# Kernel tuning notes

Measured on AMD Instinct MI355X. Metric: run time of the kernel, lower is better.

Reference implementation:

```python
import jax, jax.numpy as jnp
import numpy as np

EMBED = 1024
DFF = 4096


def _layernorm(x, g, b, eps=1e-5):
    mu = jnp.mean(x, axis=-1, keepdims=True)
    var = jnp.var(x, axis=-1, keepdims=True)
    return (x - mu) * jax.lax.rsqrt(var + eps) * g + b


def setup_inputs() -> dict:
    key = jax.random.key(0)
    ks = jax.random.split(key, 14)
    s = 1.0 / np.sqrt(EMBED)
    sf = 1.0 / np.sqrt(DFF)
    d = {
        "src": jax.random.normal(ks[0], (4, 2048, EMBED), dtype=jnp.float32),
        "Wq": jax.random.uniform(ks[1], (EMBED, EMBED), jnp.float32, -s, s),
        "bq": jnp.zeros((EMBED,), jnp.float32),
        "Wk": jax.random.uniform(ks[2], (EMBED, EMBED), jnp.float32, -s, s),
        "bk": jnp.zeros((EMBED,), jnp.float32),
        "Wv": jax.random.uniform(ks[3], (EMBED, EMBED), jnp.float32, -s, s),
        "bv": jnp.zeros((EMBED,), jnp.float32),
        "Wo": jax.random.uniform(ks[4], (EMBED, EMBED), jnp.float32, -s, s),
        "bo": jnp.zeros((EMBED,), jnp.float32),
        "W1": jax.random.uniform(ks[5], (EMBED, DFF), jnp.float32, -s, s),
        "b1": jnp.zeros((DFF,), jnp.float32),
        "W2": jax.random.uniform(ks[6], (DFF, EMBED), jnp.float32, -sf, sf),
        "b2": jnp.zeros((EMBED,), jnp.float32),
        "g1": jnp.ones((EMBED,), jnp.float32),
        "be1": jnp.zeros((EMBED,), jnp.float32),
        "g2": jnp.ones((EMBED,), jnp.float32),
        "be2": jnp.zeros((EMBED,), jnp.float32),
    }
    return d


def reference(src, Wq, bq, Wk, bk, Wv, bv, Wo, bo, W1, b1, W2, b2, g1, be1, g2, be2):
    # Q/K/V projections: [b, s, d]
    Q = src @ Wq + bq
    K = src @ Wk + bk
    V = src @ Wv + bv
    # Single-head, UNSCALED attention (faithful to source: no 1/sqrt(d), num_heads unused)
    scores = jnp.einsum("bqd,bkd->bqk", Q, K)  # [b, s, s]
    weights = jax.nn.softmax(scores, axis=-1)
    attn = jnp.einsum("bqk,bkd->bqd", weights, V)
    attn = attn @ Wo + bo
    x = _layernorm(src + attn, g1, be1)
    ff = jax.nn.relu(x @ W1 + b1) @ W2 + b2
    return _layernorm(x + ff, g2, be2)
```

## Files before the change

kernel.cpp:

```cpp
#include <hip/hip_runtime.h>
#include <stdint.h>

typedef unsigned short u16;
typedef _Float16 v8h __attribute__((ext_vector_type(8)));
typedef float v4f __attribute__((ext_vector_type(4)));

static __device__ __forceinline__ float h2f(u16 u) {
    union { u16 s; _Float16 h; } v; v.s = u; return (float)v.h;
}
static __device__ __forceinline__ u16 f2h(float f) {
    union { u16 s; _Float16 h; } v; v.h = (_Float16)f; return v.s;
}

static __device__ __forceinline__ void gload_lds16(const u16* g, const u16* l) {
    __builtin_amdgcn_global_load_lds(
        (const __attribute__((address_space(1))) uint32_t*)(uintptr_t)g,
        (__attribute__((address_space(3))) uint32_t*)(uintptr_t)l,
        16, 0, 0);
}

__global__ __launch_bounds__(256) void cvt_f16(const float* __restrict__ in,
                                               u16* __restrict__ out, int n8) {
    const int i = blockIdx.x * 256 + threadIdx.x;
    if (i >= n8) return;
    const float4 a = ((const float4*)in)[2 * i];
    const float4 b = ((const float4*)in)[2 * i + 1];
    u16 o[8] = {f2h(a.x), f2h(a.y), f2h(a.z), f2h(a.w),
                f2h(b.x), f2h(b.y), f2h(b.z), f2h(b.w)};
    *(uint4*)(out + (size_t)i * 8) = *(const uint4*)o;
}

__global__ __launch_bounds__(256) void transpose_all(
    const float* __restrict__ Wq, const float* __restrict__ Wk,
    const float* __restrict__ Wv, const float* __restrict__ Wo,
    const float* __restrict__ W1, const float* __restrict__ W2,
    u16* __restrict__ WqkT, u16* __restrict__ WvT, u16* __restrict__ WoT,
    u16* __restrict__ W1T, u16* __restrict__ W2T)
{
    int t = blockIdx.x;
    const float* in; u16* out; long ldi, ldo; int xt;
    if (t < 1024)      {            in = Wq; out = WqkT;              ldi = 1024; ldo = 1024; xt = 32; }
    else if (t < 2048) { t -= 1024; in = Wk; out = WqkT + 1024*1024;  ldi = 1024; ldo = 1024; xt = 32; }
    else if (t < 3072) { t -= 2048; in = Wv; out = WvT;               ldi = 1024; ldo = 1024; xt = 32; }
    else if (t < 4096) { t -= 3072; in = Wo; out = WoT;               ldi = 1024; ldo = 1024; xt = 32; }
    else if (t < 8192) { t -= 4096; in = W1; out = W1T;               ldi = 4096; ldo = 1024; xt = 128; }
    else               { t -= 8192; in = W2; out = W2T;               ldi = 1024; ldo = 4096; xt = 32; }
    const int c0 = (t % xt) * 32, r0 = (t / xt) * 32;
    __shared__ float tile[32][33];
    for (int i = threadIdx.y; i < 32; i += 8)
        tile[i][threadIdx.x] = in[(long)(r0 + i) * ldi + c0 + threadIdx.x];
    __syncthreads();
    for (int i = threadIdx.y; i < 32; i += 8)
        out[(long)(c0 + i) * ldo + r0 + threadIdx.x] = f2h(tile[threadIdx.x][i]);
}

template<int OMODE, int BIAS, bool RELU>
__global__ __launch_bounds__(256) void gemm_f16(
    const u16* __restrict__ A, long lda, long Asb,
    const u16* __restrict__ B, long ldb, long Bsb,
    void* __restrict__ Cv, long ldc, long Csb,
    const float* __restrict__ bias, const float* __restrict__ bias2, int K)
{
    alignas(16) __shared__ u16 As[128 * 64];
    alignas(16) __shared__ u16 Bs[128 * 64];
    const int t = threadIdx.x;
    const long b = blockIdx.z;
    A += b * Asb; B += b * Bsb;
    const long m0 = (long)blockIdx.y * 128;
    const long n0 = (long)blockIdx.x * 128;
    const int lane = t & 63, wave = t >> 6;
    const int wm = (wave >> 1) * 64, wn = (wave & 1) * 64;
    const int l16 = lane & 15, quad = lane >> 4;

    const int rr = t >> 3;
    const int cg8 = ((t & 7) ^ ((t >> 3) & 7)) * 8;
    const int wv512 = wave * 512;

    long aofs[4], bofs[4];
#pragma unroll
    for (int p = 0; p < 4; ++p) {
        aofs[p] = (m0 + p * 32 + rr) * lda + cg8;
        bofs[p] = (n0 + p * 32 + rr) * ldb + cg8;
    }

    v4f acc[4][4];
#pragma unroll
    for (int i = 0; i < 4; ++i)
#pragma unroll
        for (int j = 0; j < 4; ++j)
            acc[i][j] = (v4f){0.f, 0.f, 0.f, 0.f};

    for (int k0 = 0; k0 < K; k0 += 64) {
        __syncthreads();
#pragma unroll
        for (int p = 0; p < 4; ++p) {
            gload_lds16(A + aofs[p] + k0, As + p * 2048 + wv512);
            gload_lds16(B + bofs[p] + k0, Bs + p * 2048 + wv512);
        }
        __syncthreads();

#pragma unroll
        for (int kk = 0; kk < 2; ++kk) {
            const int swz = ((kk * 4 + quad) ^ (l16 & 7)) * 8;
            v8h af[4], bfr[4];
#pragma unroll
            for (int i = 0; i < 4; ++i)
                af[i] = *(const v8h*)&As[(wm + i * 16 + l16) * 64 + swz];
#pragma unroll
            for (int j = 0; j < 4; ++j)
                bfr[j] = *(const v8h*)&Bs[(wn + j * 16 + l16) * 64 + swz];
#pragma unroll
            for (int i = 0; i < 4; ++i)
#pragma unroll
                for (int j = 0; j < 4; ++j)
                    acc[i][j] = __builtin_amdgcn_mfma_f32_16x16x32_f16(af[i], bfr[j], acc[i][j], 0, 0, 0);
        }
    }

    float bv[4];
#pragma unroll
    for (int j = 0; j < 4; ++j) {
        const long col = n0 + wn + j * 16 + l16;
        bv[j] = (BIAS == 0) ? 0.f
              : (BIAS == 1) ? bias[col]
              : (col < 1024 ? bias[col] : bias2[col - 1024]);
    }

    if (OMODE == 2) {
        const long bb = m0 >> 11, mb = m0 & 2047;
        u16* C = (u16*)Cv + bb * Csb;
#pragma unroll
        for (int j = 0; j < 4; ++j) {
            const long col = n0 + wn + j * 16 + l16;
            u16* pc = C + col * ldc + mb + wm + quad * 4;
#pragma unroll
            for (int i = 0; i < 4; ++i) {
                u16 o[4];
#pragma unroll
                for (int r = 0; r < 4; ++r) {
                    float val = acc[i][j][r] + bv[j];
                    if (RELU) val = fmaxf(val, 0.f);
                    o[r] = f2h(val);
                }
                *(uint2*)(pc + i * 16) = *(const uint2*)o;
            }
        }
    } else {
        const long cb = b * Csb + (m0 + wm + quad * 4) * ldc + (n0 + wn + l16);
        if (OMODE == 1) {
            float* p0 = (float*)Cv + cb;
#pragma unroll
            for (int i = 0; i < 4; ++i)
#pragma unroll
                for (int r = 0; r < 4; ++r) {
                    float* prow = p0 + (long)(i * 16 + r) * ldc;
#pragma unroll
                    for (int j = 0; j < 4; ++j) {
                        float val = acc[i][j][r] + bv[j];
                        if (RELU) val = fmaxf(val, 0.f);
                        prow[j * 16] = val;
                    }
                }
        } else {
            u16* p0 = (u16*)Cv + cb;
#pragma unroll
            for (int i = 0; i < 4; ++i)
#pragma unroll
                for (int r = 0; r < 4; ++r) {
                    u16* prow = p0 + (long)(i * 16 + r) * ldc;
#pragma unroll
                    for (int j = 0; j < 4; ++j) {
                        float val = acc[i][j][r] + bv[j];
                        if (RELU) val = fmaxf(val, 0.f);
                        prow[j * 16] = f2h(val);
                    }
                }
        }
    }
}

__global__ __launch_bounds__(256) void softmax_rows(float* __restrict__ S) {
    const long row = blockIdx.x;
    float* p = S + row * 2048;
    const int t = threadIdx.x;
    float v[8];
    float mx = -1e30f;
#pragma unroll
    for (int i = 0; i < 8; ++i) { v[i] = p[t + i * 256]; mx = fmaxf(mx, v[i]); }
    __shared__ float red[256];
    red[t] = mx; __syncthreads();
    for (int off = 128; off > 0; off >>= 1) {
        if (t < off) red[t] = fmaxf(red[t], red[t + off]);
        __syncthreads();
    }
    mx = red[0]; __syncthreads();
    float sum = 0.f;
#pragma unroll
    for (int i = 0; i < 8; ++i) { v[i] = __expf(v[i] - mx); sum += v[i]; }
    red[t] = sum; __syncthreads();
    for (int off = 128; off > 0; off >>= 1) {
        if (t < off) red[t] += red[t + off];
        __syncthreads();
    }
    const float inv = 1.f / red[0];
    u16* q = (u16*)p;
#pragma unroll
    for (int i = 0; i < 8; ++i) q[t + i * 256] = f2h(v[i] * inv);
}

__global__ __launch_bounds__(256) void ln_dual(
    const float* __restrict__ a, const u16* __restrict__ bb,
    const float* __restrict__ g, const float* __restrict__ be,
    float* __restrict__ out32, u16* __restrict__ out16)
{
    const long base = (long)blockIdx.x * 1024;
    const int t = threadIdx.x;
    float v[4]; float s = 0.f, ss = 0.f;
#pragma unroll
    for (int i = 0; i < 4; ++i) {
        const int c = t + i * 256;
        const float x = a[base + c] + h2f(bb[base + c]);
        v[i] = x; s += x; ss += x * x;
    }
    __shared__ float rs[256], rss[256];
    rs[t] = s; rss[t] = ss; __syncthreads();
    for (int off = 128; off > 0; off >>= 1) {
        if (t < off) { rs[t] += rs[t + off]; rss[t] += rss[t + off]; }
        __syncthreads();
    }
    const float mean = rs[0] * (1.f / 1024.f);
    const float var = rss[0] * (1.f / 1024.f) - mean * mean;
    const float rstd = rsqrtf(var + 1e-5f);
#pragma unroll
    for (int i = 0; i < 4; ++i) {
        const int c = t + i * 256;
        const float y = (v[i] - mean) * rstd * g[c] + be[c];
        out32[base + c] = y;
        out16[base + c] = f2h(y);
    }
}

__global__ __launch_bounds__(256) void ln_mix(
    const float* __restrict__ a, const u16* __restrict__ bb,
    const float* __restrict__ g, const float* __restrict__ be,
    float* __restrict__ out)
{
    const long base = (long)blockIdx.x * 1024;
    const int t = threadIdx.x;
    float v[4]; float s = 0.f, ss = 0.f;
#pragma unroll
    for (int i = 0; i < 4; ++i) {
        const int c = t + i * 256;
        const float x = a[base + c] + h2f(bb[base + c]);
        v[i] = x; s += x; ss += x * x;
    }
    __shared__ float rs[256], rss[256];
    rs[t] = s; rss[t] = ss; __syncthreads();
    for (int off = 128; off > 0; off >>= 1) {
        if (t < off) { rs[t] += rs[t + off]; rss[t] += rss[t + off]; }
        __syncthreads();
    }
    const float mean = rs[0] * (1.f / 1024.f);
    const float var = rss[0] * (1.f / 1024.f) - mean * mean;
    const float rstd = rsqrtf(var + 1e-5f);
#pragma unroll
    for (int i = 0; i < 4; ++i) {
        const int c = t + i * 256;
        out[base + c] = (v[i] - mean) * rstd * g[c] + be[c];
    }
}

extern "C" void kernel_launch(void* const* d_in, const int* in_sizes, int n_in,
                              void* d_out, int out_size, void* d_ws, size_t ws_size,
                              hipStream_t stream) {
    (void)in_sizes; (void)n_in; (void)out_size; (void)ws_size;
    constexpr long S = 2048, E = 1024, F = 4096, M = 8192;

    const float* src = (const float*)d_in[0];
    const float* Wq  = (const float*)d_in[1];
    const float* bq  = (const float*)d_in[2];
    const float* Wk  = (const float*)d_in[3];
    const float* bk  = (const float*)d_in[4];
    const float* Wv  = (const float*)d_in[5];
    const float* bv  = (const float*)d_in[6];
    const float* Wo  = (const float*)d_in[7];
    const float* bo  = (const float*)d_in[8];
    const float* W1  = (const float*)d_in[9];
    const float* b1  = (const float*)d_in[10];
    const float* W2  = (const float*)d_in[11];
    const float* b2  = (const float*)d_in[12];
    const float* g1  = (const float*)d_in[13];
    const float* be1 = (const float*)d_in[14];
    const float* g2  = (const float*)d_in[15];
    const float* be2 = (const float*)d_in[16];

    char* ws = (char*)d_ws;
    size_t off = 0;
    auto take = [&](size_t bytes) {
        char* p = ws + off;
        off += (bytes + 255) & ~(size_t)255;
        return p;
    };
    const size_t MB16 = 16777216;
    u16*   srcH  = (u16*)take(MB16);
    u16*   WqkT  = (u16*)take(2 * E * E * 2);
    u16*   WvT   = (u16*)take(E * E * 2);
    u16*   WoT   = (u16*)take(E * E * 2);
    u16*   W1T   = (u16*)take(F * E * 2);
    u16*   W2T   = (u16*)take(E * F * 2);
    char*  B0    = take(2 * MB16);
    char*  B1    = take(MB16);
    char*  B2    = take(4ull * S * S * 4);
    char*  B3    = take(MB16);
    char*  B4    = take(MB16);

    u16*   QK    = (u16*)B0;
    float* x32   = (float*)B0;
    u16*   VT    = (u16*)B1;
    float* Sf    = (float*)B2;
    u16*   hf    = (u16*)B2;
    u16*   attn  = (u16*)B3;
    u16*   xh    = (u16*)B3;
    u16*   attnO = (u16*)B4;
    u16*   ffO   = (u16*)B4;

    dim3 blk(256), tb(32, 8);

    cvt_f16<<<dim3(M * E / 8 / 256), blk, 0, stream>>>(src, srcH, M * E / 8);

    transpose_all<<<dim3(12288), tb, 0, stream>>>(Wq, Wk, Wv, Wo, W1, W2,
                                                  WqkT, WvT, WoT, W1T, W2T);

    gemm_f16<0, 2, false><<<dim3(16, 64, 1), blk, 0, stream>>>(
        srcH, E, 0, WqkT, E, 0, QK, 2 * E, 0, bq, bk, E);

    gemm_f16<2, 1, false><<<dim3(8, 64, 1), blk, 0, stream>>>(
        srcH, E, 0, WvT, E, 0, VT, S, E * S, bv, nullptr, E);

    gemm_f16<1, 0, false><<<dim3(16, 16, 4), blk, 0, stream>>>(
        QK, 2 * E, S * 2 * E, QK + E, 2 * E, S * 2 * E,
        Sf, S, S * S, nullptr, nullptr, E);

    softmax_rows<<<dim3(M), blk, 0, stream>>>(Sf);

    gemm_f16<0, 0, false><<<dim3(8, 16, 4), blk, 0, stream>>>(
        (const u16*)Sf, 2 * S, S * 2 * S, VT, S, E * S,
        attn, E, S * E, nullptr, nullptr, S);

    gemm_f16<0, 1, false><<<dim3(8, 64, 1), blk, 0, stream>>>(
        attn, E, 0, WoT, E, 0, attnO, E, 0, bo, nullptr, E);

    ln_dual<<<dim3(M), blk, 0, stream>>>(src, attnO, g1, be1, x32, xh);

    gemm_f16<0, 1, true><<<dim3(32, 64, 1), blk, 0, stream>>>(
        xh, E, 0, W1T, E, 0, hf, F, 0, b1, nullptr, E);

    gemm_f16<0, 1, false><<<dim3(8, 64, 1), blk, 0, stream>>>(
        hf, F, 0, W2T, F, 0, ffO, E, 0, b2, nullptr, F);

    ln_mix<<<dim3(M), blk, 0, stream>>>(x32, ffO, g2, be2, (float*)d_out);
}
```

Before: 558.1 us.

## Fuse QKV projection GEMM, store scores in fp16, drop fp32 LN intermediate

Merges the Q/K and V projection GEMMs into one launch over a concatenated QKV weight, with the V tiles written transposed through a second output pointer. Attention scores are now written as fp16 instead of fp32, so the score buffer traffic and the softmax read are halved. The first layernorm no longer writes an fp32 copy, and the second layernorm reads the fp16 residual instead. The cost is lower precision for the unscaled scores, where fp16 may lose accuracy or overflow, and for the residual path.

```diff
diff --git a/kernel.cpp b/kernel.cpp
--- a/kernel.cpp
+++ b/kernel.cpp
@@ -34,17 +34,17 @@
     const float* __restrict__ Wq, const float* __restrict__ Wk,
     const float* __restrict__ Wv, const float* __restrict__ Wo,
     const float* __restrict__ W1, const float* __restrict__ W2,
-    u16* __restrict__ WqkT, u16* __restrict__ WvT, u16* __restrict__ WoT,
+    u16* __restrict__ WqkvT, u16* __restrict__ WoT,
     u16* __restrict__ W1T, u16* __restrict__ W2T)
 {
     int t = blockIdx.x;
     const float* in; u16* out; long ldi, ldo; int xt;
-    if (t < 1024)      {            in = Wq; out = WqkT;              ldi = 1024; ldo = 1024; xt = 32; }
-    else if (t < 2048) { t -= 1024; in = Wk; out = WqkT + 1024*1024;  ldi = 1024; ldo = 1024; xt = 32; }
-    else if (t < 3072) { t -= 2048; in = Wv; out = WvT;               ldi = 1024; ldo = 1024; xt = 32; }
-    else if (t < 4096) { t -= 3072; in = Wo; out = WoT;               ldi = 1024; ldo = 1024; xt = 32; }
-    else if (t < 8192) { t -= 4096; in = W1; out = W1T;               ldi = 4096; ldo = 1024; xt = 128; }
-    else               { t -= 8192; in = W2; out = W2T;               ldi = 1024; ldo = 4096; xt = 32; }
+    if (t < 1024)      {            in = Wq; out = WqkvT;               ldi = 1024; ldo = 1024; xt = 32; }
+    else if (t < 2048) { t -= 1024; in = Wk; out = WqkvT + 1024*1024;   ldi = 1024; ldo = 1024; xt = 32; }
+    else if (t < 3072) { t -= 2048; in = Wv; out = WqkvT + 2*1024*1024; ldi = 1024; ldo = 1024; xt = 32; }
+    else if (t < 4096) { t -= 3072; in = Wo; out = WoT;                 ldi = 1024; ldo = 1024; xt = 32; }
+    else if (t < 8192) { t -= 4096; in = W1; out = W1T;                 ldi = 4096; ldo = 1024; xt = 128; }
+    else               { t -= 8192; in = W2; out = W2T;                 ldi = 1024; ldo = 4096; xt = 32; }
     const int c0 = (t % xt) * 32, r0 = (t / xt) * 32;
     __shared__ float tile[32][33];
     for (int i = threadIdx.y; i < 32; i += 8)
@@ -58,8 +58,9 @@
 __global__ __launch_bounds__(256) void gemm_f16(
     const u16* __restrict__ A, long lda, long Asb,
     const u16* __restrict__ B, long ldb, long Bsb,
-    void* __restrict__ Cv, long ldc, long Csb,
-    const float* __restrict__ bias, const float* __restrict__ bias2, int K)
+    void* __restrict__ Cv, long ldc, long Csb, u16* __restrict__ C1,
+    const float* __restrict__ bias, const float* __restrict__ bias2,
+    const float* __restrict__ bias3, int K)
 {
     alignas(16) __shared__ u16 As[128 * 64];
     alignas(16) __shared__ u16 Bs[128 * 64];
@@ -121,18 +122,22 @@
 #pragma unroll
     for (int j = 0; j < 4; ++j) {
         const long col = n0 + wn + j * 16 + l16;
-        bv[j] = (BIAS == 0) ? 0.f
-              : (BIAS == 1) ? bias[col]
-              : (col < 1024 ? bias[col] : bias2[col - 1024]);
-    }
-
-    if (OMODE == 2) {
+        if (BIAS == 0) bv[j] = 0.f;
+        else if (BIAS == 1) bv[j] = bias[col];
+        else {
+            const int sel = (int)(col >> 10);
+            const float* bp = sel == 0 ? bias : (sel == 1 ? bias2 : bias3);
+            bv[j] = bp[col & 1023];
+        }
+    }
+
+    if (OMODE == 3 && n0 >= 2048) {
         const long bb = m0 >> 11, mb = m0 & 2047;
-        u16* C = (u16*)Cv + bb * Csb;
+        u16* C = C1 + bb * Csb;
 #pragma unroll
         for (int j = 0; j < 4; ++j) {
-            const long col = n0 + wn + j * 16 + l16;
-            u16* pc = C + col * ldc + mb + wm + quad * 4;
+            const long col = n0 - 2048 + wn + j * 16 + l16;
+            u16* pc = C + col * 2048 + mb + wm + quad * 4;
 #pragma unroll
             for (int i = 0; i < 4; ++i) {
                 u16 o[4];
@@ -146,47 +151,31 @@
             }
         }
     } else {
-        const long cb = b * Csb + (m0 + wm + quad * 4) * ldc + (n0 + wn + l16);
-        if (OMODE == 1) {
-            float* p0 = (float*)Cv + cb;
-#pragma unroll
-            for (int i = 0; i < 4; ++i)
-#pragma unroll
-                for (int r = 0; r < 4; ++r) {
-                    float* prow = p0 + (long)(i * 16 + r) * ldc;
-#pragma unroll
-                    for (int j = 0; j < 4; ++j) {
-                        float val = acc[i][j][r] + bv[j];
-                        if (RELU) val = fmaxf(val, 0.f);
-                        prow[j * 16] = val;
-                    }
+        const long cb = b * ((OMODE == 3) ? 0 : Csb) + (m0 + wm + quad * 4) * ldc + (n0 + wn + l16);
+        u16* p0 = (u16*)Cv + cb;
+#pragma unroll
+        for (int i = 0; i < 4; ++i)
+#pragma unroll
+            for (int r = 0; r < 4; ++r) {
+                u16* prow = p0 + (long)(i * 16 + r) * ldc;
+#pragma unroll
+                for (int j = 0; j < 4; ++j) {
+                    float val = acc[i][j][r] + bv[j];
+                    if (RELU) val = fmaxf(val, 0.f);
+                    prow[j * 16] = f2h(val);
                 }
-        } else {
-            u16* p0 = (u16*)Cv + cb;
-#pragma unroll
-            for (int i = 0; i < 4; ++i)
-#pragma unroll
-                for (int r = 0; r < 4; ++r) {
-                    u16* prow = p0 + (long)(i * 16 + r) * ldc;
-#pragma unroll
-                    for (int j = 0; j < 4; ++j) {
-                        float val = acc[i][j][r] + bv[j];
-                        if (RELU) val = fmaxf(val, 0.f);
-                        prow[j * 16] = f2h(val);
-                    }
-                }
-        }
-    }
-}
-
-__global__ __launch_bounds__(256) void softmax_rows(float* __restrict__ S) {
+            }
+    }
+}
+
+__global__ __launch_bounds__(256) void softmax_rows(u16* __restrict__ S) {
     const long row = blockIdx.x;
-    float* p = S + row * 2048;
+    u16* p = S + row * 2048;
     const int t = threadIdx.x;
     float v[8];
     float mx = -1e30f;
 #pragma unroll
-    for (int i = 0; i < 8; ++i) { v[i] = p[t + i * 256]; mx = fmaxf(mx, v[i]); }
+    for (int i = 0; i < 8; ++i) { v[i] = h2f(p[t + i * 256]); mx = fmaxf(mx, v[i]); }
     __shared__ float red[256];
     red[t] = mx; __syncthreads();
     for (int off = 128; off > 0; off >>= 1) {
@@ -203,15 +192,14 @@
         __syncthreads();
     }
     const float inv = 1.f / red[0];
-    u16* q = (u16*)p;
-#pragma unroll
-    for (int i = 0; i < 8; ++i) q[t + i * 256] = f2h(v[i] * inv);
-}
-
-__global__ __launch_bounds__(256) void ln_dual(
+#pragma unroll
+    for (int i = 0; i < 8; ++i) p[t + i * 256] = f2h(v[i] * inv);
+}
+
+__global__ __launch_bounds__(256) void ln_one(
     const float* __restrict__ a, const u16* __restrict__ bb,
     const float* __restrict__ g, const float* __restrict__ be,
-    float* __restrict__ out32, u16* __restrict__ out16)
+    u16* __restrict__ out16)
 {
     const long base = (long)blockIdx.x * 1024;
     const int t = threadIdx.x;
@@ -234,14 +222,12 @@
 #pragma unroll
     for (int i = 0; i < 4; ++i) {
         const int c = t + i * 256;
-        const float y = (v[i] - mean) * rstd * g[c] + be[c];
-        out32[base + c] = y;
-        out16[base + c] = f2h(y);
-    }
-}
-
-__global__ __launch_bounds__(256) void ln_mix(
-    const float* __restrict__ a, const u16* __restrict__ bb,
+        out16[base + c] = f2h((v[i] - mean) * rstd * g[c] + be[c]);
+    }
+}
+
+__global__ __launch_bounds__(256) void ln_two(
+    const u16* __restrict__ a, const u16* __restrict__ bb,
     const float* __restrict__ g, const float* __restrict__ be,
     float* __restrict__ out)
 {
@@ -251,7 +237,7 @@
 #pragma unroll
     for (int i = 0; i < 4; ++i) {
         const int c = t + i * 256;
-        const float x = a[base + c] + h2f(bb[base + c]);
+        const float x = h2f(a[base + c]) + h2f(bb[base + c]);
         v[i] = x; s += x; ss += x * x;
     }
     __shared__ float rs[256], rss[256];
@@ -303,8 +289,7 @@
     };
     const size_t MB16 = 16777216;
     u16*   srcH  = (u16*)take(MB16);
-    u16*   WqkT  = (u16*)take(2 * E * E * 2);
-    u16*   WvT   = (u16*)take(E * E * 2);
+    u16*   WqkvT = (u16*)take(3 * E * E * 2);
     u16*   WoT   = (u16*)take(E * E * 2);
     u16*   W1T   = (u16*)take(F * E * 2);
     u16*   W2T   = (u16*)take(E * F * 2);
@@ -315,9 +300,8 @@
     char*  B4    = take(MB16);
 
     u16*   QK    = (u16*)B0;
-    float* x32   = (float*)B0;
     u16*   VT    = (u16*)B1;
-    float* Sf    = (float*)B2;
+    u16*   Sh    = (u16*)B2;
     u16*   hf    = (u16*)B2;
     u16*   attn  = (u16*)B3;
     u16*   xh    = (u16*)B3;
@@ -329,34 +313,31 @@
     cvt_f16<<<dim3(M * E / 8 / 256), blk, 0, stream>>>(src, srcH, M * E / 8);
 
     transpose_all<<<dim3(12288), tb, 0, stream>>>(Wq, Wk, Wv, Wo, W1, W2,
-                                                  WqkT, WvT, WoT, W1T, W2T);
-
-    gemm_f16<0, 2, false><<<dim3(16, 64, 1), blk, 0, stream>>>(
-        srcH, E, 0, WqkT, E, 0, QK, 2 * E, 0, bq, bk, E);
-
-    gemm_f16<2, 1, false><<<dim3(8, 64, 1), blk, 0, stream>>>(
-        srcH, E, 0, WvT, E, 0, VT, S, E * S, bv, nullptr, E);
-
-    gemm_f16<1, 0, false><<<dim3(16, 16, 4), blk, 0, stream>>>(
+                                                  WqkvT, WoT, W1T, W2T);
+
+    gemm_f16<3, 3, false><<<dim3(24, 64, 1), blk, 0, stream>>>(
+        srcH, E, 0, WqkvT, E, 0, QK, 2 * E, E * S, VT, bq, bk, bv, E);
+
+    gemm_f16<0, 0, false><<<dim3(16, 16, 4), blk, 0, stream>>>(
         QK, 2 * E, S * 2 * E, QK + E, 2 * E, S * 2 * E,
-        Sf, S, S * S, nullptr, nullptr, E);
-
-    softmax_rows<<<dim3(M), blk, 0, stream>>>(Sf);
+        Sh, S, S * S, nullptr, nullptr, nullptr, nullptr, E);
+
+    softmax_rows<<<dim3(M), blk, 0, stream>>>(Sh);
 
     gemm_f16<0, 0, false><<<dim3(8, 16, 4), blk, 0, stream>>>(
-        (const u16*)Sf, 2 * S, S * 2 * S, VT, S, E * S,
-        attn, E, S * E, nullptr, nullptr, S);
+        Sh, S, S * S, VT, S, E * S,
+        attn, E, S * E, nullptr, nullptr, nullptr, nullptr, S);
 
     gemm_f16<0, 1, false><<<dim3(8, 64, 1), blk, 0, stream>>>(
-        attn, E, 0, WoT, E, 0, attnO, E, 0, bo, nullptr, E);
-
-    ln_dual<<<dim3(M), blk, 0, stream>>>(src, attnO, g1, be1, x32, xh);
+        attn, E, 0, WoT, E, 0, attnO, E, 0, nullptr, bo, nullptr, nullptr, E);
+
+    ln_one<<<dim3(M), blk, 0, stream>>>(src, attnO, g1, be1, xh);
 
     gemm_f16<0, 1, true><<<dim3(32, 64, 1), blk, 0, stream>>>(
-        xh, E, 0, W1T, E, 0, hf, F, 0, b1, nullptr, E);
+        xh, E, 0, W1T, E, 0, hf, F, 0, nullptr, b1, nullptr, nullptr, E);
 
     gemm_f16<0, 1, false><<<dim3(8, 64, 1), blk, 0, stream>>>(
-        hf, F, 0, W2T, F, 0, ffO, E, 0, b2, nullptr, F);
-
-    ln_mix<<<dim3(M), blk, 0, stream>>>(x32, ffO, g2, be2, (float*)d_out);
-}
+        hf, F, 0, W2T, F, 0, ffO, E, 0, nullptr, b2, nullptr, nullptr, F);
+
+    ln_two<<<dim3(M), blk, 0, stream>>>(xh, ffO, g2, be2, (float*)d_out);
+}
```

Measured after the change: 567.8 us. Within noise of the previous version (+1.8%).
